# Kernel optimization log

Measured on AMD Instinct MI355X. Metric: run time of the kernel, lower is better.

## Reference

```python
import jax, jax.numpy as jnp
import numpy as np

NUM_USERS = 100000
NUM_ITEMS = 50000
EMBED_K = 64
N_INT = 2000000
BATCH = 4096
NEG_SLOPE = 0.01  # torch F.leaky_relu default


def setup_inputs() -> dict:
    key = jax.random.key(0)
    ks = jax.random.split(key, 10)
    # xavier-uniform-like embeddings
    lim_u = float(np.sqrt(6.0 / (NUM_USERS + EMBED_K)))
    lim_i = float(np.sqrt(6.0 / (NUM_ITEMS + EMBED_K)))
    Gu = jax.random.uniform(ks[0], (NUM_USERS, EMBED_K), minval=-lim_u, maxval=lim_u, dtype=jnp.float32)
    Gi = jax.random.uniform(ks[1], (NUM_ITEMS, EMBED_K), minval=-lim_i, maxval=lim_i, dtype=jnp.float32)
    # torch Linear(2k, k): weight [k, 2k], bias [k]; Linear(k, k): [k, k]
    b1lim = float(1.0 / np.sqrt(2 * EMBED_K))
    b2lim = float(1.0 / np.sqrt(EMBED_K))
    W1 = jax.random.uniform(ks[2], (EMBED_K, 2 * EMBED_K), minval=-b1lim, maxval=b1lim, dtype=jnp.float32)
    b1 = jax.random.uniform(ks[3], (EMBED_K,), minval=-b1lim, maxval=b1lim, dtype=jnp.float32)
    W2 = jax.random.uniform(ks[4], (EMBED_K, EMBED_K), minval=-b2lim, maxval=b2lim, dtype=jnp.float32)
    b2 = jax.random.uniform(ks[5], (EMBED_K,), minval=-b2lim, maxval=b2lim, dtype=jnp.float32)
    # interaction table ui: row0 = user ids (every user appears at least once), row1 = item ids
    u_rest = jax.random.randint(ks[6], (N_INT - NUM_USERS,), 0, NUM_USERS, dtype=jnp.int32)
    ui_u = jnp.concatenate([jnp.arange(NUM_USERS, dtype=jnp.int32), u_rest])
    ui_i = jax.random.randint(ks[7], (N_INT,), 0, NUM_ITEMS, dtype=jnp.int32)
    ui = jnp.stack([ui_u, ui_i], axis=0)  # [2, N_INT]
    users = jax.random.randint(ks[8], (BATCH,), 0, NUM_USERS, dtype=jnp.int32)
    items = jax.random.randint(ks[9], (BATCH,), 0, NUM_ITEMS, dtype=jnp.int32)
    return {"Gu": Gu, "Gi": Gi, "W1": W1, "b1": b1, "W2": W2, "b2": b2,
            "users": users, "items": items, "ui": ui}


def reference(Gu, Gi, W1, b1, W2, b2, users, items, ui):
    def interaction_repr(u_emb, i_emb):
        x = jnp.concatenate([u_emb, i_emb], axis=-1)            # [., 2k]
        h = jax.nn.leaky_relu(x @ W1.T + b1, NEG_SLOPE)          # [., k]
        return h @ W2.T + b2                                     # [., k]

    u_ids, i_ids = ui[0], ui[1]
    # per-interaction representation over ALL interactions (replaces per-user loop)
    h = interaction_repr(Gu[u_ids], Gi[i_ids])                   # [N_INT, k]
    sums = jax.ops.segment_sum(h, u_ids, num_segments=NUM_USERS)             # [U, k]
    counts = jax.ops.segment_sum(jnp.ones((u_ids.shape[0],), h.dtype), u_ids,
                                 num_segments=NUM_USERS)                      # [U]
    gu_star_all = sums / jnp.maximum(counts, 1.0)[:, None]       # mean-pool per user
    gu_star = gu_star_all[users]                                 # [B, k]

    gamma_u = Gu[users]                                          # [B, k]
    gamma_i = Gi[items]                                          # [B, k]
    gui = interaction_repr(gamma_u, gamma_i)                     # [B, k]
    xui = jnp.sum(gu_star * gui, axis=1)                         # [B]
    return (xui, gu_star, gamma_i)
```

## Files before the change

### kernel.cpp

```cpp
#include <hip/hip_runtime.h>

#define U_N 100000
#define I_N 50000
#define KD 64
#define NI 2000000
#define BB 4096
#define SLOPE 0.01f
#define CHUNK 2048
#define PI_BLOCKS 782
#define GEMM_BLOCKS (PI_BLOCKS + BB / 64)
#define BIN_BLOCKS ((NI + CHUNK - 1) / CHUNK)
#define BINCAP 64



__global__ __launch_bounds__(256) void k_build(const int* __restrict__ users,
                                               const float* __restrict__ W2,
                                               unsigned int* __restrict__ map32,
                                               int* __restrict__ counts,
                                               float* __restrict__ W2T) {
    if (blockIdx.x == 16) {
        for (int idx = threadIdx.x; idx < 64 * 64; idx += 256) {
            int j = idx >> 6, k = idx & 63;
            W2T[k * 64 + j] = W2[idx];
        }
        return;
    }
    int b = blockIdx.x * 256 + threadIdx.x;
    if (b < BB) {
        counts[b] = 0;
        unsigned int u = (unsigned int)users[b];
        map32[u] = ((u + 1u) << 12) | (unsigned int)b;
    }
}

__global__ __launch_bounds__(256) void k_bulk(const float* __restrict__ Gu,
                                              const float* __restrict__ Gi,
                                              const float* __restrict__ W1,
                                              const float* __restrict__ b1,
                                              const int* __restrict__ users,
                                              const int* __restrict__ ui_u,
                                              const int* __restrict__ ui_i,
                                              const unsigned int* __restrict__ map32,
                                              float* __restrict__ PI,
                                              float* __restrict__ PUB,
                                              int* __restrict__ bins,
                                              int* __restrict__ counts) {
    __shared__ float4 wt[64 * 16];
    __shared__ float4 at[64 * 16];
    const int tid = threadIdx.x;

    if (blockIdx.x >= GEMM_BLOCKS) {
        int bid = blockIdx.x - GEMM_BLOCKS;
        int base = bid * CHUNK + tid * 8;
        if (base + 8 <= NI) {
            int4 u0 = *(const int4*)(ui_u + base);
            int4 u1 = *(const int4*)(ui_u + base + 4);
            int4 i0 = *(const int4*)(ui_i + base);
            int4 i1 = *(const int4*)(ui_i + base + 4);
            int us[8] = {u0.x, u0.y, u0.z, u0.w, u1.x, u1.y, u1.z, u1.w};
            int is[8] = {i0.x, i0.y, i0.z, i0.w, i1.x, i1.y, i1.z, i1.w};
#pragma unroll
            for (int j = 0; j < 8; ++j) {
                unsigned int e = map32[us[j]];
                if ((e >> 12) == (unsigned int)us[j] + 1u) {
                    int rep = (int)(e & 4095u);
                    int pos = atomicAdd(&counts[rep], 1);
                    if (pos < BINCAP) bins[rep * BINCAP + pos] = is[j];
                }
            }
        } else {
            for (int j = 0; j < 8; ++j) {
                int t = base + j;
                if (t < NI) {
                    unsigned int e = map32[ui_u[t]];
                    if ((e >> 12) == (unsigned int)ui_u[t] + 1u) {
                        int rep = (int)(e & 4095u);
                        int pos = atomicAdd(&counts[rep], 1);
                        if (pos < BINCAP) bins[rep * BINCAP + pos] = ui_i[t];
                    }
                }
            }
        }
        return;
    }

    const bool isPUB = (blockIdx.x >= PI_BLOCKS);
    const int base = isPUB ? (int)(blockIdx.x - PI_BLOCKS) * 64 : (int)blockIdx.x * 64;
    const int off = isPUB ? 0 : KD;

    for (int fidx = tid; fidx < 1024; fidx += 256) {
        int c = fidx >> 4, g = fidx & 15;
        wt[c * 16 + (g ^ (c >> 2))] = *(const float4*)(W1 + c * 128 + off + g * 4);
    }
    for (int fidx = tid; fidx < 1024; fidx += 256) {
        int lr = fidx >> 4, g = fidx & 15;
        int r = base + lr;
        const float* src = isPUB ? (Gu + (size_t)users[r] * KD)
                                 : (Gi + (size_t)(r < I_N ? r : I_N - 1) * KD);
        at[lr * 16 + (g ^ (lr >> 2))] = *(const float4*)(src + g * 4);
    }
    __syncthreads();

    const int ty = tid >> 4, tx = tid & 15;
    float acc[4][4];
    if (isPUB) {
        float4 bv = *(const float4*)(b1 + tx * 4);
#pragma unroll
        for (int i = 0; i < 4; ++i) {
            acc[i][0] = bv.x; acc[i][1] = bv.y; acc[i][2] = bv.z; acc[i][3] = bv.w;
        }
    } else {
#pragma unroll
        for (int i = 0; i < 4; ++i)
            for (int j = 0; j < 4; ++j) acc[i][j] = 0.0f;
    }

#pragma unroll 2
    for (int g = 0; g < 16; ++g) {
        float4 a[4], w[4];
#pragma unroll
        for (int i = 0; i < 4; ++i) a[i] = at[(ty * 4 + i) * 16 + (g ^ ty)];
#pragma unroll
        for (int j = 0; j < 4; ++j) w[j] = wt[(tx * 4 + j) * 16 + (g ^ tx)];
#pragma unroll
        for (int i = 0; i < 4; ++i)
#pragma unroll
            for (int j = 0; j < 4; ++j)
                acc[i][j] += a[i].x * w[j].x + a[i].y * w[j].y +
                             a[i].z * w[j].z + a[i].w * w[j].w;
    }

    float* outp = isPUB ? PUB : PI;
#pragma unroll
    for (int i = 0; i < 4; ++i) {
        int r = base + ty * 4 + i;
        if (!isPUB && r >= I_N) continue;
        float4 v = {acc[i][0], acc[i][1], acc[i][2], acc[i][3]};
        *(float4*)(outp + (size_t)r * KD + tx * 4) = v;
    }
}

__global__ __launch_bounds__(256) void k_final(const int* __restrict__ users,
                                               const int* __restrict__ items,
                                               const unsigned int* __restrict__ map32,
                                               const int* __restrict__ bins,
                                               const int* __restrict__ counts,
                                               const float* __restrict__ PUB,
                                               const float* __restrict__ PI,
                                               const float* __restrict__ W2T,
                                               const float* __restrict__ b2,
                                               const float* __restrict__ Gi,
                                               float* __restrict__ out) {
    __shared__ float As[4][64];
    __shared__ float Av[4][64];
    int lane = threadIdx.x & 63;
    int w = threadIdx.x >> 6;
    int b = blockIdx.x * 4 + w;

    int u = users[b];
    int rep = (int)(map32[u] & 4095u);
    int it = items[b];
    int c = counts[rep];
    int n = c < BINCAP ? c : BINCAP;
    if (c < 1) c = 1;

    float pub = PUB[(size_t)rep * KD + lane];
    const int* bl = bins + rep * BINCAP;
    float acc0 = 0.0f, acc1 = 0.0f, acc2 = 0.0f, acc3 = 0.0f;
    int e = 0;
    for (; e + 4 <= n; e += 4) {
        int itA = bl[e], itB = bl[e + 1], itC = bl[e + 2], itD = bl[e + 3];
        float vA = pub + PI[(size_t)itA * KD + lane];
        float vB = pub + PI[(size_t)itB * KD + lane];
        float vC = pub + PI[(size_t)itC * KD + lane];
        float vD = pub + PI[(size_t)itD * KD + lane];
        acc0 += (vA > 0.0f) ? vA : vA * SLOPE;
        acc1 += (vB > 0.0f) ? vB : vB * SLOPE;
        acc2 += (vC > 0.0f) ? vC : vC * SLOPE;
        acc3 += (vD > 0.0f) ? vD : vD * SLOPE;
    }
    for (; e < n; ++e) {
        float v = pub + PI[(size_t)bl[e] * KD + lane];
        acc0 += (v > 0.0f) ? v : v * SLOPE;
    }
    float A = ((acc0 + acc1) + (acc2 + acc3)) / (float)c;

    float av = pub + PI[(size_t)it * KD + lane];
    av = (av > 0.0f) ? av : av * SLOPE;

    As[w][lane] = A;
    Av[w][lane] = av;

    float gu = b2[lane];
    float gi = b2[lane];
#pragma unroll
    for (int g = 0; g < 16; ++g) {
        float4 a4 = *(const float4*)&As[w][g * 4];
        float4 v4 = *(const float4*)&Av[w][g * 4];
#pragma unroll
        for (int t = 0; t < 4; ++t) {
            float wv = W2T[(g * 4 + t) * 64 + lane];
            float aa = t == 0 ? a4.x : t == 1 ? a4.y : t == 2 ? a4.z : a4.w;
            float vv = t == 0 ? v4.x : t == 1 ? v4.y : t == 2 ? v4.z : v4.w;
            gu += aa * wv;
            gi += vv * wv;
        }
    }

    float prod = gu * gi;
#pragma unroll
    for (int off = 32; off > 0; off >>= 1) prod += __shfl_down(prod, off);

    if (lane == 0) out[b] = prod;
    out[(size_t)BB + (size_t)b * KD + lane] = gu;
    out[(size_t)BB + (size_t)BB * KD + (size_t)b * KD + lane] =
        Gi[(size_t)it * KD + lane];
}


extern "C" void kernel_launch(void* const* d_in, const int* in_sizes, int n_in,
                              void* d_out, int out_size, void* d_ws, size_t ws_size,
                              hipStream_t stream) {
    const float* Gu = (const float*)d_in[0];
    const float* Gi = (const float*)d_in[1];
    const float* W1 = (const float*)d_in[2];
    const float* b1 = (const float*)d_in[3];
    const float* W2 = (const float*)d_in[4];
    const float* b2 = (const float*)d_in[5];
    const int* users = (const int*)d_in[6];
    const int* items = (const int*)d_in[7];
    const int* ui = (const int*)d_in[8];
    const int* ui_u = ui;
    const int* ui_i = ui + NI;
    float* out = (float*)d_out;

    char* ws = (char*)d_ws;
    size_t off = 0;
    unsigned int* map32 = (unsigned int*)(ws + off); off += 400128;
    float* PI = (float*)(ws + off);    off += 12800000;
    float* PUB = (float*)(ws + off);   off += 1048576;
    int* counts = (int*)(ws + off);    off += 16384;
    int* bins = (int*)(ws + off);      off += (size_t)BB * BINCAP * 4;
    float* W2T = (float*)(ws + off);   off += 16384;

    k_build<<<17, 256, 0, stream>>>(users, W2, map32, counts, W2T);

    k_bulk<<<GEMM_BLOCKS + BIN_BLOCKS, 256, 0, stream>>>(
        Gu, Gi, W1, b1, users, ui_u, ui_i, map32, PI, PUB, bins, counts);

    k_final<<<BB / 4, 256, 0, stream>>>(users, items, map32, bins, counts, PUB, PI, W2T, b2, Gi, out);
}
```

Baseline: 43.18 us.

## Use bf16 MFMA for first-layer projection GEMM instead of FP32 LDS tiling

Replaces the shared-memory tiled FP32 FMA GEMM in k_bulk with per-wave bf16 MFMA 16x16x32 instructions. Embedding rows are converted to bf16 in registers and W1 is pre-converted to bf16 once in k_build. This removes the LDS staging and the barrier and makes the projection compute-cheap. The cost is reduced precision from bf16 inputs and less coalesced scalar output stores.

Result: slower. 47.70 us (+10.5%).

```diff
diff --git a/kernel.cpp b/kernel.cpp
--- a/kernel.cpp
+++ b/kernel.cpp
@@ -12,18 +12,42 @@
 #define BIN_BLOCKS ((NI + CHUNK - 1) / CHUNK)
 #define BINCAP 64
 
+typedef __attribute__((ext_vector_type(8))) short short8;
+typedef __attribute__((ext_vector_type(4))) float f32x4;
+
+__device__ inline unsigned short f2bf(float f) {
+    unsigned int b = __float_as_uint(f);
+    b += 0x7fffu + ((b >> 16) & 1u);
+    return (unsigned short)(b >> 16);
+}
+
+__device__ inline short8 load_bf8(const float* p) {
+    float4 x = *(const float4*)p;
+    float4 y = *(const float4*)(p + 4);
+    short8 r;
+    r[0] = (short)f2bf(x.x); r[1] = (short)f2bf(x.y);
+    r[2] = (short)f2bf(x.z); r[3] = (short)f2bf(x.w);
+    r[4] = (short)f2bf(y.x); r[5] = (short)f2bf(y.y);
+    r[6] = (short)f2bf(y.z); r[7] = (short)f2bf(y.w);
+    return r;
+}
+
 
 
 __global__ __launch_bounds__(256) void k_build(const int* __restrict__ users,
                                                const float* __restrict__ W2,
+                                               const float* __restrict__ W1,
                                                unsigned int* __restrict__ map32,
                                                int* __restrict__ counts,
-                                               float* __restrict__ W2T) {
+                                               float* __restrict__ W2T,
+                                               unsigned short* __restrict__ W1bf) {
     if (blockIdx.x == 16) {
         for (int idx = threadIdx.x; idx < 64 * 64; idx += 256) {
             int j = idx >> 6, k = idx & 63;
             W2T[k * 64 + j] = W2[idx];
         }
+        for (int idx = threadIdx.x; idx < 64 * 128; idx += 256)
+            W1bf[idx] = f2bf(W1[idx]);
         return;
     }
     int b = blockIdx.x * 256 + threadIdx.x;
@@ -36,7 +60,7 @@
 
 __global__ __launch_bounds__(256) void k_bulk(const float* __restrict__ Gu,
                                               const float* __restrict__ Gi,
-                                              const float* __restrict__ W1,
+                                              const unsigned short* __restrict__ W1bf,
                                               const float* __restrict__ b1,
                                               const int* __restrict__ users,
                                               const int* __restrict__ ui_u,
@@ -46,8 +70,6 @@
                                               float* __restrict__ PUB,
                                               int* __restrict__ bins,
                                               int* __restrict__ counts) {
-    __shared__ float4 wt[64 * 16];
-    __shared__ float4 at[64 * 16];
     const int tid = threadIdx.x;
 
     if (blockIdx.x >= GEMM_BLOCKS) {
@@ -86,58 +108,49 @@
     }
 
     const bool isPUB = (blockIdx.x >= PI_BLOCKS);
-    const int base = isPUB ? (int)(blockIdx.x - PI_BLOCKS) * 64 : (int)blockIdx.x * 64;
+    const int blkbase = isPUB ? (int)(blockIdx.x - PI_BLOCKS) * 64
+                              : (int)blockIdx.x * 64;
     const int off = isPUB ? 0 : KD;
-
-    for (int fidx = tid; fidx < 1024; fidx += 256) {
-        int c = fidx >> 4, g = fidx & 15;
-        wt[c * 16 + (g ^ (c >> 2))] = *(const float4*)(W1 + c * 128 + off + g * 4);
-    }
-    for (int fidx = tid; fidx < 1024; fidx += 256) {
-        int lr = fidx >> 4, g = fidx & 15;
-        int r = base + lr;
-        const float* src = isPUB ? (Gu + (size_t)users[r] * KD)
-                                 : (Gi + (size_t)(r < I_N ? r : I_N - 1) * KD);
-        at[lr * 16 + (g ^ (lr >> 2))] = *(const float4*)(src + g * 4);
-    }
-    __syncthreads();
-
-    const int ty = tid >> 4, tx = tid & 15;
-    float acc[4][4];
+    const int l = tid & 63;
+    const int wid = tid >> 6;
+    const int m = l & 15, hi = l >> 4;
+    const int rowbase = blkbase + wid * 16;
+
+    const float* rowp;
     if (isPUB) {
-        float4 bv = *(const float4*)(b1 + tx * 4);
-#pragma unroll
-        for (int i = 0; i < 4; ++i) {
-            acc[i][0] = bv.x; acc[i][1] = bv.y; acc[i][2] = bv.z; acc[i][3] = bv.w;
-        }
+        rowp = Gu + (size_t)users[rowbase + m] * KD;
     } else {
-#pragma unroll
-        for (int i = 0; i < 4; ++i)
-            for (int j = 0; j < 4; ++j) acc[i][j] = 0.0f;
-    }
-
-#pragma unroll 2
-    for (int g = 0; g < 16; ++g) {
-        float4 a[4], w[4];
-#pragma unroll
-        for (int i = 0; i < 4; ++i) a[i] = at[(ty * 4 + i) * 16 + (g ^ ty)];
-#pragma unroll
-        for (int j = 0; j < 4; ++j) w[j] = wt[(tx * 4 + j) * 16 + (g ^ tx)];
-#pragma unroll
-        for (int i = 0; i < 4; ++i)
-#pragma unroll
-            for (int j = 0; j < 4; ++j)
-                acc[i][j] += a[i].x * w[j].x + a[i].y * w[j].y +
-                             a[i].z * w[j].z + a[i].w * w[j].w;
+        int r = rowbase + m; if (r >= I_N) r = I_N - 1;
+        rowp = Gi + (size_t)r * KD;
+    }
+    short8 a0 = load_bf8(rowp + hi * 8);
+    short8 a1 = load_bf8(rowp + 32 + hi * 8);
+
+    f32x4 acc[4];
+#pragma unroll
+    for (int ct = 0; ct < 4; ++ct) {
+        float bv = isPUB ? b1[ct * 16 + m] : 0.0f;
+        acc[ct] = f32x4{bv, bv, bv, bv};
+    }
+
+#pragma unroll
+    for (int ct = 0; ct < 4; ++ct) {
+        const unsigned short* wrow = W1bf + (ct * 16 + m) * 128 + off + hi * 8;
+        short8 w0 = *(const short8*)wrow;
+        short8 w1 = *(const short8*)(wrow + 32);
+        acc[ct] = __builtin_amdgcn_mfma_f32_16x16x32_bf16(a0, w0, acc[ct], 0, 0, 0);
+        acc[ct] = __builtin_amdgcn_mfma_f32_16x16x32_bf16(a1, w1, acc[ct], 0, 0, 0);
     }
 
     float* outp = isPUB ? PUB : PI;
 #pragma unroll
-    for (int i = 0; i < 4; ++i) {
-        int r = base + ty * 4 + i;
-        if (!isPUB && r >= I_N) continue;
-        float4 v = {acc[i][0], acc[i][1], acc[i][2], acc[i][3]};
-        *(float4*)(outp + (size_t)r * KD + tx * 4) = v;
+    for (int ct = 0; ct < 4; ++ct) {
+#pragma unroll
+        for (int reg = 0; reg < 4; ++reg) {
+            int r = rowbase + hi * 4 + reg;
+            if (!isPUB && r >= I_N) continue;
+            outp[(size_t)r * KD + ct * 16 + m] = acc[ct][reg];
+        }
     }
 }
 
@@ -243,11 +256,12 @@
     int* counts = (int*)(ws + off);    off += 16384;
     int* bins = (int*)(ws + off);      off += (size_t)BB * BINCAP * 4;
     float* W2T = (float*)(ws + off);   off += 16384;
-
-    k_build<<<17, 256, 0, stream>>>(users, W2, map32, counts, W2T);
+    unsigned short* W1bf = (unsigned short*)(ws + off); off += 16384;
+
+    k_build<<<17, 256, 0, stream>>>(users, W2, W1, map32, counts, W2T, W1bf);
 
     k_bulk<<<GEMM_BLOCKS + BIN_BLOCKS, 256, 0, stream>>>(
-        Gu, Gi, W1, b1, users, ui_u, ui_i, map32, PI, PUB, bins, counts);
+        Gu, Gi, W1bf, b1, users, ui_u, ui_i, map32, PI, PUB, bins, counts);
 
     k_final<<<BB / 4, 256, 0, stream>>>(users, items, map32, bins, counts, PUB, PI, W2T, b2, Gi, out);
 }
```

## Regroup kernels: fuse build into GEMM kernel, split binning into own kernel

Applied to the files above, without the earlier changes.

The small map/counts build and W2 transpose now run as extra blocks inside the projection GEMM kernel, and the interaction binning pass moves out to a separate kernel that runs after it. Previously the build kernel ran alone and the GEMM and binning blocks shared one launch. The launch count stays at three. The likely aim is to hide the tiny build work behind the GEMM and give the atomic-heavy binning a launch of its own. The cost is that binning can no longer overlap with the GEMM blocks.

New measurement: 47.75 us. 10.6% more time.

```diff
diff --git a/kernel.cpp b/kernel.cpp
--- a/kernel.cpp
+++ b/kernel.cpp
@@ -8,85 +8,48 @@
 #define SLOPE 0.01f
 #define CHUNK 2048
 #define PI_BLOCKS 782
+#define BUILD_BLOCKS 17
 #define GEMM_BLOCKS (PI_BLOCKS + BB / 64)
 #define BIN_BLOCKS ((NI + CHUNK - 1) / CHUNK)
 #define BINCAP 64
 
 
 
-__global__ __launch_bounds__(256) void k_build(const int* __restrict__ users,
-                                               const float* __restrict__ W2,
-                                               unsigned int* __restrict__ map32,
-                                               int* __restrict__ counts,
-                                               float* __restrict__ W2T) {
-    if (blockIdx.x == 16) {
-        for (int idx = threadIdx.x; idx < 64 * 64; idx += 256) {
-            int j = idx >> 6, k = idx & 63;
-            W2T[k * 64 + j] = W2[idx];
-        }
-        return;
-    }
-    int b = blockIdx.x * 256 + threadIdx.x;
-    if (b < BB) {
-        counts[b] = 0;
-        unsigned int u = (unsigned int)users[b];
-        map32[u] = ((u + 1u) << 12) | (unsigned int)b;
-    }
-}
-
-__global__ __launch_bounds__(256) void k_bulk(const float* __restrict__ Gu,
-                                              const float* __restrict__ Gi,
-                                              const float* __restrict__ W1,
-                                              const float* __restrict__ b1,
-                                              const int* __restrict__ users,
-                                              const int* __restrict__ ui_u,
-                                              const int* __restrict__ ui_i,
-                                              const unsigned int* __restrict__ map32,
-                                              float* __restrict__ PI,
-                                              float* __restrict__ PUB,
-                                              int* __restrict__ bins,
-                                              int* __restrict__ counts) {
+__global__ __launch_bounds__(256) void k_gemmbuild(const float* __restrict__ Gu,
+                                                   const float* __restrict__ Gi,
+                                                   const float* __restrict__ W1,
+                                                   const float* __restrict__ b1,
+                                                   const float* __restrict__ W2,
+                                                   const int* __restrict__ users,
+                                                   unsigned int* __restrict__ map32,
+                                                   int* __restrict__ counts,
+                                                   float* __restrict__ W2T,
+                                                   float* __restrict__ PI,
+                                                   float* __restrict__ PUB) {
     __shared__ float4 wt[64 * 16];
     __shared__ float4 at[64 * 16];
     const int tid = threadIdx.x;
 
-    if (blockIdx.x >= GEMM_BLOCKS) {
-        int bid = blockIdx.x - GEMM_BLOCKS;
-        int base = bid * CHUNK + tid * 8;
-        if (base + 8 <= NI) {
-            int4 u0 = *(const int4*)(ui_u + base);
-            int4 u1 = *(const int4*)(ui_u + base + 4);
-            int4 i0 = *(const int4*)(ui_i + base);
-            int4 i1 = *(const int4*)(ui_i + base + 4);
-            int us[8] = {u0.x, u0.y, u0.z, u0.w, u1.x, u1.y, u1.z, u1.w};
-            int is[8] = {i0.x, i0.y, i0.z, i0.w, i1.x, i1.y, i1.z, i1.w};
-#pragma unroll
-            for (int j = 0; j < 8; ++j) {
-                unsigned int e = map32[us[j]];
-                if ((e >> 12) == (unsigned int)us[j] + 1u) {
-                    int rep = (int)(e & 4095u);
-                    int pos = atomicAdd(&counts[rep], 1);
-                    if (pos < BINCAP) bins[rep * BINCAP + pos] = is[j];
-                }
+    if (blockIdx.x < BUILD_BLOCKS) {
+        if (blockIdx.x == 16) {
+            for (int idx = tid; idx < 64 * 64; idx += 256) {
+                int j = idx >> 6, k = idx & 63;
+                W2T[k * 64 + j] = W2[idx];
             }
         } else {
-            for (int j = 0; j < 8; ++j) {
-                int t = base + j;
-                if (t < NI) {
-                    unsigned int e = map32[ui_u[t]];
-                    if ((e >> 12) == (unsigned int)ui_u[t] + 1u) {
-                        int rep = (int)(e & 4095u);
-                        int pos = atomicAdd(&counts[rep], 1);
-                        if (pos < BINCAP) bins[rep * BINCAP + pos] = ui_i[t];
-                    }
-                }
+            int b = blockIdx.x * 256 + tid;
+            if (b < BB) {
+                counts[b] = 0;
+                unsigned int u = (unsigned int)users[b];
+                map32[u] = ((u + 1u) << 12) | (unsigned int)b;
             }
         }
         return;
     }
 
-    const bool isPUB = (blockIdx.x >= PI_BLOCKS);
-    const int base = isPUB ? (int)(blockIdx.x - PI_BLOCKS) * 64 : (int)blockIdx.x * 64;
+    const int gblk = blockIdx.x - BUILD_BLOCKS;
+    const bool isPUB = (gblk >= PI_BLOCKS);
+    const int base = isPUB ? (gblk - PI_BLOCKS) * 64 : gblk * 64;
     const int off = isPUB ? 0 : KD;
 
     for (int fidx = tid; fidx < 1024; fidx += 256) {
@@ -138,6 +101,44 @@
         if (!isPUB && r >= I_N) continue;
         float4 v = {acc[i][0], acc[i][1], acc[i][2], acc[i][3]};
         *(float4*)(outp + (size_t)r * KD + tx * 4) = v;
+    }
+}
+
+__global__ __launch_bounds__(256) void k_bin(const int* __restrict__ ui_u,
+                                             const int* __restrict__ ui_i,
+                                             const unsigned int* __restrict__ map32,
+                                             int* __restrict__ bins,
+                                             int* __restrict__ counts) {
+    const int tid = threadIdx.x;
+    int base = blockIdx.x * CHUNK + tid * 8;
+    if (base + 8 <= NI) {
+        int4 u0 = *(const int4*)(ui_u + base);
+        int4 u1 = *(const int4*)(ui_u + base + 4);
+        int4 i0 = *(const int4*)(ui_i + base);
+        int4 i1 = *(const int4*)(ui_i + base + 4);
+        int us[8] = {u0.x, u0.y, u0.z, u0.w, u1.x, u1.y, u1.z, u1.w};
+        int is[8] = {i0.x, i0.y, i0.z, i0.w, i1.x, i1.y, i1.z, i1.w};
+#pragma unroll
+        for (int j = 0; j < 8; ++j) {
+            unsigned int e = map32[us[j]];
+            if ((e >> 12) == (unsigned int)us[j] + 1u) {
+                int rep = (int)(e & 4095u);
+                int pos = atomicAdd(&counts[rep], 1);
+                if (pos < BINCAP) bins[rep * BINCAP + pos] = is[j];
+            }
+        }
+    } else {
+        for (int j = 0; j < 8; ++j) {
+            int t = base + j;
+            if (t < NI) {
+                unsigned int e = map32[ui_u[t]];
+                if ((e >> 12) == (unsigned int)ui_u[t] + 1u) {
+                    int rep = (int)(e & 4095u);
+                    int pos = atomicAdd(&counts[rep], 1);
+                    if (pos < BINCAP) bins[rep * BINCAP + pos] = ui_i[t];
+                }
+            }
+        }
     }
 }
 
@@ -244,10 +245,10 @@
     int* bins = (int*)(ws + off);      off += (size_t)BB * BINCAP * 4;
     float* W2T = (float*)(ws + off);   off += 16384;
 
-    k_build<<<17, 256, 0, stream>>>(users, W2, map32, counts, W2T);
-
-    k_bulk<<<GEMM_BLOCKS + BIN_BLOCKS, 256, 0, stream>>>(
-        Gu, Gi, W1, b1, users, ui_u, ui_i, map32, PI, PUB, bins, counts);
+    k_gemmbuild<<<BUILD_BLOCKS + GEMM_BLOCKS, 256, 0, stream>>>(
+        Gu, Gi, W1, b1, W2, users, map32, counts, W2T, PI, PUB);
+
+    k_bin<<<BIN_BLOCKS, 256, 0, stream>>>(ui_u, ui_i, map32, bins, counts);
 
     k_final<<<BB / 4, 256, 0, stream>>>(users, items, map32, bins, counts, PUB, PI, W2T, b2, Gi, out);
 }
```
